# Kernel tuning notes

Hardware: AMD Instinct MI355X
Metric: run time of the kernel (lower is better)

## Reference

```python
import jax, jax.numpy as jnp
import numpy as np

NUM_USERS = 100000
NUM_ITEMS = 100000
DIM = 128
B = 8192
H = 200
ATTN_HID = 64


def setup_inputs() -> dict:
    key = jax.random.key(0)
    ks = jax.random.split(key, 10)
    user_ids = jax.random.randint(ks[0], (B,), 0, NUM_USERS)
    item_ids = jax.random.randint(ks[1], (B,), 0, NUM_ITEMS)
    user_history = jax.random.randint(ks[2], (B, H), 0, NUM_ITEMS)
    user_table = jax.random.normal(ks[3], (NUM_USERS, DIM), dtype=jnp.float32)
    item_table = jax.random.normal(ks[4], (NUM_ITEMS, DIM), dtype=jnp.float32)
    feature_interaction = jax.random.normal(ks[5], (DIM, DIM), dtype=jnp.float32)
    # attention MLP: Linear(2*DIM, 64) -> ReLU -> Linear(64, 1) -> Sigmoid
    lim1 = 1.0 / np.sqrt(2 * DIM)
    w1 = jax.random.uniform(ks[6], (2 * DIM, ATTN_HID), minval=-lim1, maxval=lim1, dtype=jnp.float32)
    b1 = jax.random.uniform(ks[7], (ATTN_HID,), minval=-lim1, maxval=lim1, dtype=jnp.float32)
    lim2 = 1.0 / np.sqrt(ATTN_HID)
    w2 = jax.random.uniform(ks[8], (ATTN_HID, 1), minval=-lim2, maxval=lim2, dtype=jnp.float32)
    b2 = jax.random.uniform(ks[9], (1,), minval=-lim2, maxval=lim2, dtype=jnp.float32)
    return {
        "user_ids": user_ids,
        "item_ids": item_ids,
        "user_history": user_history,
        "user_table": user_table,
        "item_table": item_table,
        "feature_interaction": feature_interaction,
        "w1": w1,
        "b1": b1,
        "w2": w2,
        "b2": b2,
    }


def reference(user_ids, item_ids, user_history, user_table, item_table,
              feature_interaction, w1, b1, w2, b2):
    user_emb = user_table[user_ids]          # [B, D]
    item_emb = item_table[item_ids]          # [B, D]
    # bilinear interaction: (user_emb @ W) . item_emb, summed over D -> [B, 1]
    interaction = jnp.sum((user_emb @ feature_interaction) * item_emb, axis=1, keepdims=True)
    # attention-weighted history pooling
    history_emb = item_table[user_history]   # [B, H, D]
    u = jnp.broadcast_to(user_emb[:, None, :], history_emb.shape)  # [B, H, D]
    attn_in = jnp.concatenate([u, history_emb], axis=-1)           # [B, H, 2D]
    h = jax.nn.relu(attn_in @ w1 + b1)                             # [B, H, 64]
    attn_w = jax.nn.sigmoid(h @ w2 + b2)                           # [B, H, 1]
    history_repr = jnp.sum(attn_w * history_emb, axis=1)           # [B, D]
    user_out = user_emb + history_repr
    return (user_out, item_emb, interaction)
```

## Files before the change

### kernel.cpp

```cpp
#include <hip/hip_runtime.h>
#include <math.h>

#define NB      8192
#define HLEN    200
#define DIM     128
#define AH      64
#define NITEMS  100000
#define WTILES  7
#define GATHER_BLKS (NB / 2)
#define INTER_BLKS  (NB / 4)
#define CONV_BLKS 1024

typedef __attribute__((ext_vector_type(4))) float f32x4;
typedef __attribute__((ext_vector_type(2))) float f32x2;
typedef __attribute__((ext_vector_type(4))) int   i32x4;
typedef __attribute__((ext_vector_type(8))) short bf16x8;
typedef unsigned int uint;

__device__ __forceinline__ unsigned short f2bf(float f) {
  uint u = __float_as_uint(f);
  u += 0x7fffu + ((u >> 16) & 1u);
  return (unsigned short)(u >> 16);
}
__device__ __forceinline__ float bf2f(unsigned short h) {
  return __uint_as_float(((uint)h) << 16);
}
__device__ __forceinline__ long pick64(const i32x4& v, int h) {
  return (long)(unsigned)v[2 * h] | ((long)(unsigned)v[2 * h + 1] << 32);
}

__global__ __launch_bounds__(256)
void conv_kernel(const float* __restrict__ item_table,
                 const float* __restrict__ w1,
                 unsigned char* __restrict__ tbl8,
                 unsigned char* __restrict__ w1f8) {
  const long t0 = (long)blockIdx.x * 256 + threadIdx.x;
  const long total4 = (long)NITEMS * DIM / 4;
  const long stride = (long)CONV_BLKS * 256;
  for (long i = t0; i < total4; i += stride) {
    f32x4 v = ((const f32x4*)item_table)[i];
    int p = __builtin_amdgcn_cvt_pk_fp8_f32(v[0], v[1], 0, false);
    p     = __builtin_amdgcn_cvt_pk_fp8_f32(v[2], v[3], p, true);
    ((int*)tbl8)[i] = p;
  }
  if (t0 < 16384) {
    int L = (int)t0;
    int j = L & 7, gg = (L >> 3) & 3, mm = (L >> 5) & 15;
    int nt = (L >> 9) & 3, s = (L >> 11) & 3, part = (L >> 13) & 1;
    int kg = part * 128 + (s >> 1) * 64 + gg * 16 + (s & 1) * 8 + j;
    float v = w1[kg * AH + nt * 16 + mm];
    int pk = __builtin_amdgcn_cvt_pk_fp8_f32(v, v, 0, false);
    w1f8[L] = (unsigned char)(pk & 0xff);
  }
}

__global__ __launch_bounds__(256)
void main_kernel_fp8(const int* __restrict__ user_ids,
                     const int* __restrict__ item_ids,
                     const int* __restrict__ user_history,
                     const float* __restrict__ user_table,
                     const float* __restrict__ item_table,
                     const float* __restrict__ fi,
                     const unsigned char* __restrict__ tbl8,
                     const unsigned char* __restrict__ w1f8,
                     const float* __restrict__ b1,
                     const float* __restrict__ w2,
                     const float* __restrict__ b2,
                     float* __restrict__ out_user,
                     float* __restrict__ out_item,
                     float* __restrict__ out_inter) {
  __shared__ __align__(16) unsigned char ldsbuf[35392];
  const int t = threadIdx.x;
  if (blockIdx.x < GATHER_BLKS) {
    float* comb = (float*)ldsbuf;
    const int lane = t & 63;
    const int wave = t >> 6;
    const int bslot = wave >> 1;
    const int h = wave & 1;
    const int b = blockIdx.x * 2 + bslot;
    const int m = lane & 15;
    const int g = lane >> 4;

    const int uid = __builtin_amdgcn_readfirstlane(user_ids[b]);
    const float* urow = user_table + (long)uid * DIM;
    const int* hrow = user_history + (long)b * HLEN;

    int idxs[WTILES];
#pragma unroll
    for (int tt = 0; tt < WTILES; ++tt) {
      int row = (h * WTILES + tt) * 16 + m;
      idxs[tt] = (row < HLEN) ? hrow[row] : 0;
    }

    i32x4 pa[4][2];
#define LOADT(T, BUF)                                                          \
    {                                                                          \
      const unsigned char* p_ = tbl8 + ((long)idxs[T] << 7) + g * 16;          \
      pa[BUF][0] = *(const i32x4*)p_;                                          \
      pa[BUF][1] = *(const i32x4*)(p_ + 64);                                   \
    }
    LOADT(0, 0) LOADT(1, 1) LOADT(2, 2)

    i32x4 uf[2];
#pragma unroll
    for (int kb = 0; kb < 2; ++kb) {
      const float* up = urow + kb * 64 + g * 16;
      f32x4 q0 = *(const f32x4*)(up + 0);
      f32x4 q1 = *(const f32x4*)(up + 4);
      f32x4 q2 = *(const f32x4*)(up + 8);
      f32x4 q3 = *(const f32x4*)(up + 12);
      i32x4 d;
      d[0] = __builtin_amdgcn_cvt_pk_fp8_f32(q0[0], q0[1], 0, false);
      d[0] = __builtin_amdgcn_cvt_pk_fp8_f32(q0[2], q0[3], d[0], true);
      d[1] = __builtin_amdgcn_cvt_pk_fp8_f32(q1[0], q1[1], 0, false);
      d[1] = __builtin_amdgcn_cvt_pk_fp8_f32(q1[2], q1[3], d[1], true);
      d[2] = __builtin_amdgcn_cvt_pk_fp8_f32(q2[0], q2[1], 0, false);
      d[2] = __builtin_amdgcn_cvt_pk_fp8_f32(q2[2], q2[3], d[2], true);
      d[3] = __builtin_amdgcn_cvt_pk_fp8_f32(q3[0], q3[1], 0, false);
      d[3] = __builtin_amdgcn_cvt_pk_fp8_f32(q3[2], q3[3], d[3], true);
      uf[kb] = d;
    }

    const unsigned char* wtop = w1f8;
    const unsigned char* wbot = w1f8 + 8192;

    f32x4 accu[4];
#pragma unroll
    for (int nt = 0; nt < 4; ++nt) accu[nt] = (f32x4){0.f, 0.f, 0.f, 0.f};
#pragma unroll
    for (int s = 0; s < 4; ++s) {
      long a_s = pick64(uf[s >> 1], s & 1);
#pragma unroll
      for (int nt = 0; nt < 4; ++nt) {
        long bf = *(const long*)(wtop + ((s * 4 + nt) * 16 + m) * 32 + g * 8);
        accu[nt] = __builtin_amdgcn_mfma_f32_16x16x32_fp8_fp8(a_s, bf, accu[nt], 0, 0, 0);
      }
    }
    float ubreg[4], w2reg[4];
#pragma unroll
    for (int nt = 0; nt < 4; ++nt) {
      ubreg[nt] = accu[nt][0] + b1[nt * 16 + m];
      w2reg[nt] = w2[nt * 16 + m];
    }
    const float b2v = b2[0];

    long bfr[4][4];
#pragma unroll
    for (int s = 0; s < 4; ++s)
#pragma unroll
      for (int nt = 0; nt < 4; ++nt)
        bfr[s][nt] = *(const long*)(wbot + ((s * 4 + nt) * 16 + m) * 32 + g * 8);

    float arep[32];
#pragma unroll
    for (int c = 0; c < 32; ++c) arep[c] = 0.f;

#pragma unroll
    for (int tt = 0; tt < WTILES; ++tt) {
      if (tt + 3 < WTILES) LOADT(tt + 3, (tt + 3) & 3)
      const int cb = tt & 3;

      f32x4 acc[4];
#pragma unroll
      for (int nt = 0; nt < 4; ++nt) acc[nt] = (f32x4){0.f, 0.f, 0.f, 0.f};
#pragma unroll
      for (int s = 0; s < 4; ++s) {
        long a_s = pick64(pa[cb][s >> 1], s & 1);
#pragma unroll
        for (int nt = 0; nt < 4; ++nt)
          acc[nt] = __builtin_amdgcn_mfma_f32_16x16x32_fp8_fp8(a_s, bfr[s][nt], acc[nt], 0, 0, 0);
      }

      float sums[4];
#pragma unroll
      for (int r = 0; r < 4; ++r) {
        float s = 0.f;
#pragma unroll
        for (int nt = 0; nt < 4; ++nt) {
          float hh = fmaxf(acc[nt][r] + ubreg[nt], 0.f);
          s = fmaf(hh, w2reg[nt], s);
        }
        s += __shfl_xor(s, 1);
        s += __shfl_xor(s, 2);
        s += __shfl_xor(s, 4);
        s += __shfl_xor(s, 8);
        sums[r] = s;
      }
      const int q = m & 3;
      float keep = (q == 0) ? sums[0] : (q == 1) ? sums[1] : (q == 2) ? sums[2] : sums[3];
      float sv = __shfl(keep, ((m >> 2) << 4) | m);
      float attw = 1.f / (1.f + __expf(-(sv + b2v)));
      if ((h * WTILES + tt) * 16 + m >= HLEN) attw = 0.f;

#pragma unroll
      for (int kb = 0; kb < 2; ++kb)
#pragma unroll
        for (int d = 0; d < 4; ++d) {
          f32x2 lo = __builtin_amdgcn_cvt_pk_f32_fp8(pa[cb][kb][d], false);
          f32x2 hi = __builtin_amdgcn_cvt_pk_f32_fp8(pa[cb][kb][d], true);
          const int base = kb * 16 + d * 4;
          arep[base + 0] = fmaf(attw, lo[0], arep[base + 0]);
          arep[base + 1] = fmaf(attw, lo[1], arep[base + 1]);
          arep[base + 2] = fmaf(attw, hi[0], arep[base + 2]);
          arep[base + 3] = fmaf(attw, hi[1], arep[base + 3]);
        }
    }
#undef LOADT

#pragma unroll
    for (int c = 0; c < 32; ++c) {
      arep[c] += __shfl_xor(arep[c], 1);
      arep[c] += __shfl_xor(arep[c], 2);
      arep[c] += __shfl_xor(arep[c], 4);
      arep[c] += __shfl_xor(arep[c], 8);
    }

    if (h == 1 && m == 0) {
#pragma unroll
      for (int kb = 0; kb < 2; ++kb)
#pragma unroll
        for (int i4 = 0; i4 < 4; ++i4)
#pragma unroll
          for (int qq = 0; qq < 4; ++qq)
            comb[bslot * 128 + kb * 64 + g * 16 + i4 * 4 + qq] = arep[kb * 16 + i4 * 4 + qq];
    }
    __syncthreads();
    if (h == 0 && m == 0) {
#pragma unroll
      for (int kb = 0; kb < 2; ++kb)
#pragma unroll
        for (int i4 = 0; i4 < 4; ++i4) {
          const int col = kb * 64 + g * 16 + i4 * 4;
          f32x4 uv = *(const f32x4*)(urow + col);
          f32x4 o;
#pragma unroll
          for (int qq = 0; qq < 4; ++qq)
            o[qq] = uv[qq] + arep[kb * 16 + i4 * 4 + qq] + comb[bslot * 128 + col + qq];
          *(f32x4*)(out_user + (long)b * DIM + col) = o;
        }
    }
  } else {
    unsigned short* fitb = (unsigned short*)ldsbuf;
    float (*u4)[DIM] = (float(*)[DIM])(ldsbuf + 33280);
    float (*red)[4] = (float(*)[4])(ldsbuf + 35328);
    for (int i = t; i < DIM * DIM; i += 256) {
      int d = i >> 7, e = i & 127;
      fitb[e * 130 + d] = f2bf(fi[i]);
    }
    const int col = t & 127;
    const int dh = t >> 7;
    const int lane = t & 63;
    const int wv = t >> 6;
    const int bb = (blockIdx.x - GATHER_BLKS) * 4;
    for (int i = t; i < 4 * DIM; i += 256) {
      int bi = i >> 7, d = i & 127;
      u4[bi][d] = user_table[(long)user_ids[bb + bi] * DIM + d];
    }
    __syncthreads();
    const unsigned short* fr = &fitb[col * 130 + dh * 64];
    float a0 = 0.f, a1 = 0.f, a2 = 0.f, a3 = 0.f;
#pragma unroll 4
    for (int d = 0; d < 64; d += 4) {
      float f0 = bf2f(fr[d]), f1 = bf2f(fr[d + 1]), f2 = bf2f(fr[d + 2]), f3 = bf2f(fr[d + 3]);
      f32x4 q0 = *(const f32x4*)&u4[0][dh * 64 + d];
      f32x4 q1 = *(const f32x4*)&u4[1][dh * 64 + d];
      f32x4 q2 = *(const f32x4*)&u4[2][dh * 64 + d];
      f32x4 q3 = *(const f32x4*)&u4[3][dh * 64 + d];
      a0 = fmaf(f0, q0[0], a0); a0 = fmaf(f1, q0[1], a0); a0 = fmaf(f2, q0[2], a0); a0 = fmaf(f3, q0[3], a0);
      a1 = fmaf(f0, q1[0], a1); a1 = fmaf(f1, q1[1], a1); a1 = fmaf(f2, q1[2], a1); a1 = fmaf(f3, q1[3], a1);
      a2 = fmaf(f0, q2[0], a2); a2 = fmaf(f1, q2[1], a2); a2 = fmaf(f2, q2[2], a2); a2 = fmaf(f3, q2[3], a2);
      a3 = fmaf(f0, q3[0], a3); a3 = fmaf(f1, q3[1], a3); a3 = fmaf(f2, q3[2], a3); a3 = fmaf(f3, q3[3], a3);
    }
    const float vv0 = item_table[(long)item_ids[bb + 0] * DIM + col];
    const float vv1 = item_table[(long)item_ids[bb + 1] * DIM + col];
    const float vv2 = item_table[(long)item_ids[bb + 2] * DIM + col];
    const float vv3 = item_table[(long)item_ids[bb + 3] * DIM + col];
    if (dh == 0) {
      out_item[(long)(bb + 0) * DIM + col] = vv0;
      out_item[(long)(bb + 1) * DIM + col] = vv1;
      out_item[(long)(bb + 2) * DIM + col] = vv2;
      out_item[(long)(bb + 3) * DIM + col] = vv3;
    }
    float p0 = a0 * vv0, p1 = a1 * vv1, p2 = a2 * vv2, p3 = a3 * vv3;
#pragma unroll
    for (int msk = 1; msk <= 32; msk <<= 1) {
      p0 += __shfl_xor(p0, msk);
      p1 += __shfl_xor(p1, msk);
      p2 += __shfl_xor(p2, msk);
      p3 += __shfl_xor(p3, msk);
    }
    if (lane == 0) { red[wv][0] = p0; red[wv][1] = p1; red[wv][2] = p2; red[wv][3] = p3; }
    __syncthreads();
    if (t < 4)
      out_inter[bb + t] = red[0][t] + red[1][t] + red[2][t] + red[3][t];
  }
}

__global__ __launch_bounds__(256)
void main_fallback(const int* __restrict__ user_ids,
                   const int* __restrict__ user_history,
                   const float* __restrict__ user_table,
                   const float* __restrict__ item_table,
                   const float* __restrict__ w1,
                   const float* __restrict__ b1,
                   const float* __restrict__ w2,
                   const float* __restrict__ b2,
                   float* __restrict__ out_user) {
  const int lane = threadIdx.x & 63;
  const int wave = threadIdx.x >> 6;
  const int b = blockIdx.x * 4 + wave;
  const int m = lane & 15, g = lane >> 4;
  const int uid = __builtin_amdgcn_readfirstlane(user_ids[b]);
  const float* urow = user_table + (long)uid * DIM;
  float upj = b1[lane];
#pragma unroll 8
  for (int d = 0; d < DIM; ++d) upj = fmaf(urow[d], w1[d * AH + lane], upj);
  bf16x8 bfr[4][4];
#pragma unroll
  for (int ks = 0; ks < 4; ++ks)
#pragma unroll
    for (int nt = 0; nt < 4; ++nt) {
      bf16x8 bv;
#pragma unroll
      for (int j = 0; j < 8; ++j)
        bv[j] = (short)f2bf(w1[(DIM + ks * 32 + g * 8 + j) * AH + nt * 16 + m]);
      bfr[ks][nt] = bv;
    }
  float ubreg[4], w2reg[4];
#pragma unroll
  for (int nt = 0; nt < 4; ++nt) {
    ubreg[nt] = __shfl(upj, nt * 16 + m);
    w2reg[nt] = w2[nt * 16 + m];
  }
  const float b2v = b2[0];
  float arep[32];
#pragma unroll
  for (int c = 0; c < 32; ++c) arep[c] = 0.f;
  const int* hrow = user_history + (long)b * HLEN;
  for (int tt = 0; tt < 13; ++tt) {
    const int row = tt * 16 + m;
    const int idx = (row < HLEN) ? hrow[row] : 0;
    bf16x8 a[4];
    const float* rp = item_table + (long)idx * DIM;
#pragma unroll
    for (int ks = 0; ks < 4; ++ks) {
      f32x4 lo = *(const f32x4*)(rp + ks * 32 + g * 8);
      f32x4 hi = *(const f32x4*)(rp + ks * 32 + g * 8 + 4);
      bf16x8 av;
      av[0] = (short)f2bf(lo[0]); av[1] = (short)f2bf(lo[1]);
      av[2] = (short)f2bf(lo[2]); av[3] = (short)f2bf(lo[3]);
      av[4] = (short)f2bf(hi[0]); av[5] = (short)f2bf(hi[1]);
      av[6] = (short)f2bf(hi[2]); av[7] = (short)f2bf(hi[3]);
      a[ks] = av;
    }
    f32x4 acc[4];
#pragma unroll
    for (int nt = 0; nt < 4; ++nt) acc[nt] = (f32x4){0.f, 0.f, 0.f, 0.f};
#pragma unroll
    for (int ks = 0; ks < 4; ++ks)
#pragma unroll
      for (int nt = 0; nt < 4; ++nt)
        acc[nt] = __builtin_amdgcn_mfma_f32_16x16x32_bf16(a[ks], bfr[ks][nt], acc[nt], 0, 0, 0);
    float sums[4];
#pragma unroll
    for (int r = 0; r < 4; ++r) {
      float s = 0.f;
#pragma unroll
      for (int nt = 0; nt < 4; ++nt) {
        float hh = fmaxf(acc[nt][r] + ubreg[nt], 0.f);
        s = fmaf(hh, w2reg[nt], s);
      }
      s += __shfl_xor(s, 1); s += __shfl_xor(s, 2);
      s += __shfl_xor(s, 4); s += __shfl_xor(s, 8);
      sums[r] = s;
    }
    const int q = m & 3;
    float keep = (q == 0) ? sums[0] : (q == 1) ? sums[1] : (q == 2) ? sums[2] : sums[3];
    float sv = __shfl(keep, ((m >> 2) << 4) | m);
    float attw = 1.f / (1.f + __expf(-(sv + b2v)));
    if (row >= HLEN) attw = 0.f;
#pragma unroll
    for (int ks = 0; ks < 4; ++ks)
#pragma unroll
      for (int j = 0; j < 8; ++j)
        arep[ks * 8 + j] = fmaf(attw, bf2f((unsigned short)a[ks][j]), arep[ks * 8 + j]);
  }
#pragma unroll
  for (int c = 0; c < 32; ++c) {
    arep[c] += __shfl_xor(arep[c], 1);
    arep[c] += __shfl_xor(arep[c], 2);
    arep[c] += __shfl_xor(arep[c], 4);
    arep[c] += __shfl_xor(arep[c], 8);
  }
  if (m == 0) {
#pragma unroll
    for (int ks = 0; ks < 4; ++ks)
#pragma unroll
      for (int j = 0; j < 8; ++j) {
        const int col = ks * 32 + g * 8 + j;
        out_user[(long)b * DIM + col] = urow[col] + arep[ks * 8 + j];
      }
  }
}

__global__ __launch_bounds__(256)
void inter_kernel(const int* __restrict__ user_ids,
                  const int* __restrict__ item_ids,
                  const float* __restrict__ user_table,
                  const float* __restrict__ item_table,
                  const float* __restrict__ fi,
                  float* __restrict__ out_item,
                  float* __restrict__ out_inter) {
  __shared__ unsigned short fitb[DIM * 130];
  __shared__ float u4[4][DIM];
  __shared__ float red[4][4];
  const int t = threadIdx.x;
  for (int i = t; i < DIM * DIM; i += 256) {
    int d = i >> 7, e = i & 127;
    fitb[e * 130 + d] = f2bf(fi[i]);
  }
  const int col = t & 127;
  const int dh = t >> 7;
  const int lane = t & 63;
  const int wv = t >> 6;
  const int bb = blockIdx.x * 4;
  for (int i = t; i < 4 * DIM; i += 256) {
    int bi = i >> 7, d = i & 127;
    u4[bi][d] = user_table[(long)user_ids[bb + bi] * DIM + d];
  }
  __syncthreads();
  const unsigned short* fr = &fitb[col * 130 + dh * 64];
  float a0 = 0.f, a1 = 0.f, a2 = 0.f, a3 = 0.f;
#pragma unroll 4
  for (int d = 0; d < 64; d += 4) {
    float f0 = bf2f(fr[d]), f1 = bf2f(fr[d + 1]), f2 = bf2f(fr[d + 2]), f3 = bf2f(fr[d + 3]);
    f32x4 q0 = *(const f32x4*)&u4[0][dh * 64 + d];
    f32x4 q1 = *(const f32x4*)&u4[1][dh * 64 + d];
    f32x4 q2 = *(const f32x4*)&u4[2][dh * 64 + d];
    f32x4 q3 = *(const f32x4*)&u4[3][dh * 64 + d];
    a0 = fmaf(f0, q0[0], a0); a0 = fmaf(f1, q0[1], a0); a0 = fmaf(f2, q0[2], a0); a0 = fmaf(f3, q0[3], a0);
    a1 = fmaf(f0, q1[0], a1); a1 = fmaf(f1, q1[1], a1); a1 = fmaf(f2, q1[2], a1); a1 = fmaf(f3, q1[3], a1);
    a2 = fmaf(f0, q2[0], a2); a2 = fmaf(f1, q2[1], a2); a2 = fmaf(f2, q2[2], a2); a2 = fmaf(f3, q2[3], a2);
    a3 = fmaf(f0, q3[0], a3); a3 = fmaf(f1, q3[1], a3); a3 = fmaf(f2, q3[2], a3); a3 = fmaf(f3, q3[3], a3);
  }
  const float vv0 = item_table[(long)item_ids[bb + 0] * DIM + col];
  const float vv1 = item_table[(long)item_ids[bb + 1] * DIM + col];
  const float vv2 = item_table[(long)item_ids[bb + 2] * DIM + col];
  const float vv3 = item_table[(long)item_ids[bb + 3] * DIM + col];
  if (dh == 0) {
    out_item[(long)(bb + 0) * DIM + col] = vv0;
    out_item[(long)(bb + 1) * DIM + col] = vv1;
    out_item[(long)(bb + 2) * DIM + col] = vv2;
    out_item[(long)(bb + 3) * DIM + col] = vv3;
  }
  float p0 = a0 * vv0, p1 = a1 * vv1, p2 = a2 * vv2, p3 = a3 * vv3;
#pragma unroll
  for (int msk = 1; msk <= 32; msk <<= 1) {
    p0 += __shfl_xor(p0, msk);
    p1 += __shfl_xor(p1, msk);
    p2 += __shfl_xor(p2, msk);
    p3 += __shfl_xor(p3, msk);
  }
  if (lane == 0) { red[wv][0] = p0; red[wv][1] = p1; red[wv][2] = p2; red[wv][3] = p3; }
  __syncthreads();
  if (t < 4)
    out_inter[bb + t] = red[0][t] + red[1][t] + red[2][t] + red[3][t];
}

extern "C" void kernel_launch(void* const* d_in, const int* in_sizes, int n_in,
                              void* d_out, int out_size, void* d_ws, size_t ws_size,
                              hipStream_t stream) {
  const int*   user_ids     = (const int*)d_in[0];
  const int*   item_ids     = (const int*)d_in[1];
  const int*   user_history = (const int*)d_in[2];
  const float* user_table   = (const float*)d_in[3];
  const float* item_table   = (const float*)d_in[4];
  const float* fi           = (const float*)d_in[5];
  const float* w1           = (const float*)d_in[6];
  const float* b1           = (const float*)d_in[7];
  const float* w2           = (const float*)d_in[8];
  const float* b2           = (const float*)d_in[9];

  float* out       = (float*)d_out;
  float* out_user  = out;
  float* out_item  = out + (size_t)NB * DIM;
  float* out_inter = out + (size_t)2 * NB * DIM;

  const size_t need = (size_t)NITEMS * DIM + 16384;
  if (ws_size >= need) {
    unsigned char* tbl8 = (unsigned char*)d_ws;
    unsigned char* w1f8 = tbl8 + (size_t)NITEMS * DIM;
    conv_kernel<<<CONV_BLKS, 256, 0, stream>>>(item_table, w1, tbl8, w1f8);
    main_kernel_fp8<<<GATHER_BLKS + INTER_BLKS, 256, 0, stream>>>(user_ids, item_ids,
        user_history, user_table, item_table, fi, tbl8, w1f8, b1, w2, b2,
        out_user, out_item, out_inter);
  } else {
    main_fallback<<<NB / 4, 256, 0, stream>>>(user_ids, user_history, user_table,
        item_table, w1, b1, w2, b2, out_user);
    inter_kernel<<<NB / 4, 256, 0, stream>>>(user_ids, item_ids, user_table,
        item_table, fi, out_item, out_inter);
  }
}
```

Measured before the change: 101.5 us.

## Partition history gather by item range so blocks hit localized table slices

The history pooling is split into four item-range partitions. Each block handles one partition for four batch rows, builds a compacted list of history slots whose item falls in that range, and writes bf16 partial sums that a new reduce kernel combines with the user embedding. The intent is to keep each block's fp8 table reads within a quarter of the table for better L2/MALL locality. The user-side attention projection (user_emb @ w1_top + b1) moves into the prep kernel as scalar FMA work, and the conversion and interaction work are fused into that prep launch. The cost is an extra kernel launch, a workspace round trip through bf16 partials that loses some precision, variable tile counts per wave, and a scalar, non-MFMA projection loop.

```diff
diff --git a/kernel.cpp b/kernel.cpp
--- a/kernel.cpp
+++ b/kernel.cpp
@@ -6,10 +6,10 @@
 #define DIM     128
 #define AH      64
 #define NITEMS  100000
-#define WTILES  7
-#define GATHER_BLKS (NB / 2)
-#define INTER_BLKS  (NB / 4)
+#define NPART   4
+#define PITEMS  25000
 #define CONV_BLKS 1024
+#define INTER_BLKS (NB / 4)
 
 typedef __attribute__((ext_vector_type(4))) float f32x4;
 typedef __attribute__((ext_vector_type(2))) float f32x2;
@@ -30,214 +30,47 @@
 }
 
 __global__ __launch_bounds__(256)
-void conv_kernel(const float* __restrict__ item_table,
+void prep_kernel(const int* __restrict__ user_ids,
+                 const int* __restrict__ item_ids,
+                 const float* __restrict__ user_table,
+                 const float* __restrict__ item_table,
+                 const float* __restrict__ fi,
                  const float* __restrict__ w1,
+                 const float* __restrict__ b1,
                  unsigned char* __restrict__ tbl8,
-                 unsigned char* __restrict__ w1f8) {
-  const long t0 = (long)blockIdx.x * 256 + threadIdx.x;
-  const long total4 = (long)NITEMS * DIM / 4;
-  const long stride = (long)CONV_BLKS * 256;
-  for (long i = t0; i < total4; i += stride) {
-    f32x4 v = ((const f32x4*)item_table)[i];
-    int p = __builtin_amdgcn_cvt_pk_fp8_f32(v[0], v[1], 0, false);
-    p     = __builtin_amdgcn_cvt_pk_fp8_f32(v[2], v[3], p, true);
-    ((int*)tbl8)[i] = p;
-  }
-  if (t0 < 16384) {
-    int L = (int)t0;
-    int j = L & 7, gg = (L >> 3) & 3, mm = (L >> 5) & 15;
-    int nt = (L >> 9) & 3, s = (L >> 11) & 3, part = (L >> 13) & 1;
-    int kg = part * 128 + (s >> 1) * 64 + gg * 16 + (s & 1) * 8 + j;
-    float v = w1[kg * AH + nt * 16 + mm];
-    int pk = __builtin_amdgcn_cvt_pk_fp8_f32(v, v, 0, false);
-    w1f8[L] = (unsigned char)(pk & 0xff);
-  }
-}
-
-__global__ __launch_bounds__(256)
-void main_kernel_fp8(const int* __restrict__ user_ids,
-                     const int* __restrict__ item_ids,
-                     const int* __restrict__ user_history,
-                     const float* __restrict__ user_table,
-                     const float* __restrict__ item_table,
-                     const float* __restrict__ fi,
-                     const unsigned char* __restrict__ tbl8,
-                     const unsigned char* __restrict__ w1f8,
-                     const float* __restrict__ b1,
-                     const float* __restrict__ w2,
-                     const float* __restrict__ b2,
-                     float* __restrict__ out_user,
-                     float* __restrict__ out_item,
-                     float* __restrict__ out_inter) {
+                 unsigned char* __restrict__ w1f8,
+                 float* __restrict__ ub,
+                 float* __restrict__ out_item,
+                 float* __restrict__ out_inter) {
   __shared__ __align__(16) unsigned char ldsbuf[35392];
   const int t = threadIdx.x;
-  if (blockIdx.x < GATHER_BLKS) {
-    float* comb = (float*)ldsbuf;
-    const int lane = t & 63;
-    const int wave = t >> 6;
-    const int bslot = wave >> 1;
-    const int h = wave & 1;
-    const int b = blockIdx.x * 2 + bslot;
-    const int m = lane & 15;
-    const int g = lane >> 4;
-
-    const int uid = __builtin_amdgcn_readfirstlane(user_ids[b]);
-    const float* urow = user_table + (long)uid * DIM;
-    const int* hrow = user_history + (long)b * HLEN;
-
-    int idxs[WTILES];
-#pragma unroll
-    for (int tt = 0; tt < WTILES; ++tt) {
-      int row = (h * WTILES + tt) * 16 + m;
-      idxs[tt] = (row < HLEN) ? hrow[row] : 0;
-    }
-
-    i32x4 pa[4][2];
-#define LOADT(T, BUF)                                                          \
-    {                                                                          \
-      const unsigned char* p_ = tbl8 + ((long)idxs[T] << 7) + g * 16;          \
-      pa[BUF][0] = *(const i32x4*)p_;                                          \
-      pa[BUF][1] = *(const i32x4*)(p_ + 64);                                   \
-    }
-    LOADT(0, 0) LOADT(1, 1) LOADT(2, 2)
-
-    i32x4 uf[2];
-#pragma unroll
-    for (int kb = 0; kb < 2; ++kb) {
-      const float* up = urow + kb * 64 + g * 16;
-      f32x4 q0 = *(const f32x4*)(up + 0);
-      f32x4 q1 = *(const f32x4*)(up + 4);
-      f32x4 q2 = *(const f32x4*)(up + 8);
-      f32x4 q3 = *(const f32x4*)(up + 12);
-      i32x4 d;
-      d[0] = __builtin_amdgcn_cvt_pk_fp8_f32(q0[0], q0[1], 0, false);
-      d[0] = __builtin_amdgcn_cvt_pk_fp8_f32(q0[2], q0[3], d[0], true);
-      d[1] = __builtin_amdgcn_cvt_pk_fp8_f32(q1[0], q1[1], 0, false);
-      d[1] = __builtin_amdgcn_cvt_pk_fp8_f32(q1[2], q1[3], d[1], true);
-      d[2] = __builtin_amdgcn_cvt_pk_fp8_f32(q2[0], q2[1], 0, false);
-      d[2] = __builtin_amdgcn_cvt_pk_fp8_f32(q2[2], q2[3], d[2], true);
-      d[3] = __builtin_amdgcn_cvt_pk_fp8_f32(q3[0], q3[1], 0, false);
-      d[3] = __builtin_amdgcn_cvt_pk_fp8_f32(q3[2], q3[3], d[3], true);
-      uf[kb] = d;
-    }
-
-    const unsigned char* wtop = w1f8;
-    const unsigned char* wbot = w1f8 + 8192;
-
-    f32x4 accu[4];
-#pragma unroll
-    for (int nt = 0; nt < 4; ++nt) accu[nt] = (f32x4){0.f, 0.f, 0.f, 0.f};
-#pragma unroll
-    for (int s = 0; s < 4; ++s) {
-      long a_s = pick64(uf[s >> 1], s & 1);
-#pragma unroll
-      for (int nt = 0; nt < 4; ++nt) {
-        long bf = *(const long*)(wtop + ((s * 4 + nt) * 16 + m) * 32 + g * 8);
-        accu[nt] = __builtin_amdgcn_mfma_f32_16x16x32_fp8_fp8(a_s, bf, accu[nt], 0, 0, 0);
-      }
-    }
-    float ubreg[4], w2reg[4];
-#pragma unroll
-    for (int nt = 0; nt < 4; ++nt) {
-      ubreg[nt] = accu[nt][0] + b1[nt * 16 + m];
-      w2reg[nt] = w2[nt * 16 + m];
-    }
-    const float b2v = b2[0];
-
-    long bfr[4][4];
-#pragma unroll
-    for (int s = 0; s < 4; ++s)
-#pragma unroll
-      for (int nt = 0; nt < 4; ++nt)
-        bfr[s][nt] = *(const long*)(wbot + ((s * 4 + nt) * 16 + m) * 32 + g * 8);
-
-    float arep[32];
-#pragma unroll
-    for (int c = 0; c < 32; ++c) arep[c] = 0.f;
-
-#pragma unroll
-    for (int tt = 0; tt < WTILES; ++tt) {
-      if (tt + 3 < WTILES) LOADT(tt + 3, (tt + 3) & 3)
-      const int cb = tt & 3;
-
-      f32x4 acc[4];
-#pragma unroll
-      for (int nt = 0; nt < 4; ++nt) acc[nt] = (f32x4){0.f, 0.f, 0.f, 0.f};
-#pragma unroll
-      for (int s = 0; s < 4; ++s) {
-        long a_s = pick64(pa[cb][s >> 1], s & 1);
-#pragma unroll
-        for (int nt = 0; nt < 4; ++nt)
-          acc[nt] = __builtin_amdgcn_mfma_f32_16x16x32_fp8_fp8(a_s, bfr[s][nt], acc[nt], 0, 0, 0);
-      }
-
-      float sums[4];
-#pragma unroll
-      for (int r = 0; r < 4; ++r) {
-        float s = 0.f;
-#pragma unroll
-        for (int nt = 0; nt < 4; ++nt) {
-          float hh = fmaxf(acc[nt][r] + ubreg[nt], 0.f);
-          s = fmaf(hh, w2reg[nt], s);
-        }
-        s += __shfl_xor(s, 1);
-        s += __shfl_xor(s, 2);
-        s += __shfl_xor(s, 4);
-        s += __shfl_xor(s, 8);
-        sums[r] = s;
-      }
-      const int q = m & 3;
-      float keep = (q == 0) ? sums[0] : (q == 1) ? sums[1] : (q == 2) ? sums[2] : sums[3];
-      float sv = __shfl(keep, ((m >> 2) << 4) | m);
-      float attw = 1.f / (1.f + __expf(-(sv + b2v)));
-      if ((h * WTILES + tt) * 16 + m >= HLEN) attw = 0.f;
-
-#pragma unroll
-      for (int kb = 0; kb < 2; ++kb)
-#pragma unroll
-        for (int d = 0; d < 4; ++d) {
-          f32x2 lo = __builtin_amdgcn_cvt_pk_f32_fp8(pa[cb][kb][d], false);
-          f32x2 hi = __builtin_amdgcn_cvt_pk_f32_fp8(pa[cb][kb][d], true);
-          const int base = kb * 16 + d * 4;
-          arep[base + 0] = fmaf(attw, lo[0], arep[base + 0]);
-          arep[base + 1] = fmaf(attw, lo[1], arep[base + 1]);
-          arep[base + 2] = fmaf(attw, hi[0], arep[base + 2]);
-          arep[base + 3] = fmaf(attw, hi[1], arep[base + 3]);
-        }
-    }
-#undef LOADT
-
-#pragma unroll
-    for (int c = 0; c < 32; ++c) {
-      arep[c] += __shfl_xor(arep[c], 1);
-      arep[c] += __shfl_xor(arep[c], 2);
-      arep[c] += __shfl_xor(arep[c], 4);
-      arep[c] += __shfl_xor(arep[c], 8);
-    }
-
-    if (h == 1 && m == 0) {
-#pragma unroll
-      for (int kb = 0; kb < 2; ++kb)
-#pragma unroll
-        for (int i4 = 0; i4 < 4; ++i4)
-#pragma unroll
-          for (int qq = 0; qq < 4; ++qq)
-            comb[bslot * 128 + kb * 64 + g * 16 + i4 * 4 + qq] = arep[kb * 16 + i4 * 4 + qq];
-    }
-    __syncthreads();
-    if (h == 0 && m == 0) {
-#pragma unroll
-      for (int kb = 0; kb < 2; ++kb)
-#pragma unroll
-        for (int i4 = 0; i4 < 4; ++i4) {
-          const int col = kb * 64 + g * 16 + i4 * 4;
-          f32x4 uv = *(const f32x4*)(urow + col);
-          f32x4 o;
-#pragma unroll
-          for (int qq = 0; qq < 4; ++qq)
-            o[qq] = uv[qq] + arep[kb * 16 + i4 * 4 + qq] + comb[bslot * 128 + col + qq];
-          *(f32x4*)(out_user + (long)b * DIM + col) = o;
-        }
+  if (blockIdx.x < CONV_BLKS) {
+    const long t0 = (long)blockIdx.x * 256 + t;
+    const long total4 = (long)NITEMS * DIM / 4;
+    const long stride = (long)CONV_BLKS * 256;
+    for (long i = t0; i < total4; i += stride) {
+      f32x4 v = ((const f32x4*)item_table)[i];
+      int p = __builtin_amdgcn_cvt_pk_fp8_f32(v[0], v[1], 0, false);
+      p     = __builtin_amdgcn_cvt_pk_fp8_f32(v[2], v[3], p, true);
+      ((int*)tbl8)[i] = p;
+    }
+    if (t0 < 16384) {
+      int L = (int)t0;
+      int j = L & 7, gg = (L >> 3) & 3, mm = (L >> 5) & 15;
+      int nt = (L >> 9) & 3, s = (L >> 11) & 3, part = (L >> 13) & 1;
+      int kg = part * 128 + (s >> 1) * 64 + gg * 16 + (s & 1) * 8 + j;
+      float v = w1[kg * AH + nt * 16 + mm];
+      int pk = __builtin_amdgcn_cvt_pk_fp8_f32(v, v, 0, false);
+      w1f8[L] = (unsigned char)(pk & 0xff);
+    }
+    for (long i = t0; i < (long)NB * AH; i += stride) {
+      int b = (int)(i >> 6), n = (int)(i & 63);
+      const float* urow = user_table + (long)user_ids[b] * DIM;
+      float acc = b1[n];
+#pragma unroll 8
+      for (int d = 0; d < DIM; ++d)
+        acc = fmaf(urow[d], w1[d * AH + n], acc);
+      ub[i] = acc;
     }
   } else {
     unsigned short* fitb = (unsigned short*)ldsbuf;
@@ -251,7 +84,7 @@
     const int dh = t >> 7;
     const int lane = t & 63;
     const int wv = t >> 6;
-    const int bb = (blockIdx.x - GATHER_BLKS) * 4;
+    const int bb = (blockIdx.x - CONV_BLKS) * 4;
     for (int i = t; i < 4 * DIM; i += 256) {
       int bi = i >> 7, d = i & 127;
       u4[bi][d] = user_table[(long)user_ids[bb + bi] * DIM + d];
@@ -294,6 +127,165 @@
     if (t < 4)
       out_inter[bb + t] = red[0][t] + red[1][t] + red[2][t] + red[3][t];
   }
+}
+
+__global__ __launch_bounds__(256)
+void gather_kernel(const int* __restrict__ user_ids,
+                   const int* __restrict__ user_history,
+                   const unsigned char* __restrict__ tbl8,
+                   const unsigned char* __restrict__ w1f8,
+                   const float* __restrict__ ub,
+                   const float* __restrict__ w2,
+                   const float* __restrict__ b2,
+                   unsigned short* __restrict__ partial) {
+  __shared__ unsigned char lists[4][256];
+  const int lane = threadIdx.x & 63;
+  const int wave = threadIdx.x >> 6;
+  const int p = blockIdx.x & 3;
+  const int b = (blockIdx.x >> 2) * 4 + wave;
+  const int m = lane & 15;
+  const int g = lane >> 4;
+  const int* hrow = user_history + (long)b * HLEN;
+
+  int cnt = 0;
+#pragma unroll
+  for (int c = 0; c < 4; ++c) {
+    const int slot = c * 64 + lane;
+    const bool vld = slot < HLEN;
+    int idx = 0;
+    if (vld) idx = hrow[slot];
+    const bool inp = vld && (idx / PITEMS == p);
+    unsigned long long mask = __ballot(inp);
+    int pos = cnt + __popcll(mask & ((1ull << lane) - 1ull));
+    if (inp) lists[wave][pos] = (unsigned char)slot;
+    cnt += (int)__popcll(mask);
+  }
+  __syncthreads();
+
+  const unsigned char* wbot = w1f8 + 8192;
+  long bfr[4][4];
+#pragma unroll
+  for (int s = 0; s < 4; ++s)
+#pragma unroll
+    for (int nt = 0; nt < 4; ++nt)
+      bfr[s][nt] = *(const long*)(wbot + ((s * 4 + nt) * 16 + m) * 32 + g * 8);
+  float ubreg[4], w2reg[4];
+#pragma unroll
+  for (int nt = 0; nt < 4; ++nt) {
+    ubreg[nt] = ub[(long)b * AH + nt * 16 + m];
+    w2reg[nt] = w2[nt * 16 + m];
+  }
+  const float b2v = b2[0];
+
+  float arep[32];
+#pragma unroll
+  for (int c = 0; c < 32; ++c) arep[c] = 0.f;
+
+  const int ntiles = (cnt + 15) >> 4;
+  for (int tt = 0; tt < ntiles; ++tt) {
+    const int j = tt * 16 + m;
+    const bool valid = j < cnt;
+    int idx = 0;
+    if (valid) idx = hrow[lists[wave][j]];
+    const unsigned char* rp = tbl8 + ((long)idx << 7) + g * 16;
+    i32x4 pa0 = *(const i32x4*)rp;
+    i32x4 pa1 = *(const i32x4*)(rp + 64);
+
+    f32x4 acc[4];
+#pragma unroll
+    for (int nt = 0; nt < 4; ++nt) acc[nt] = (f32x4){0.f, 0.f, 0.f, 0.f};
+#pragma unroll
+    for (int s = 0; s < 4; ++s) {
+      long a_s = pick64((s < 2) ? pa0 : pa1, s & 1);
+#pragma unroll
+      for (int nt = 0; nt < 4; ++nt)
+        acc[nt] = __builtin_amdgcn_mfma_f32_16x16x32_fp8_fp8(a_s, bfr[s][nt], acc[nt], 0, 0, 0);
+    }
+
+    float sums[4];
+#pragma unroll
+    for (int r = 0; r < 4; ++r) {
+      float s = 0.f;
+#pragma unroll
+      for (int nt = 0; nt < 4; ++nt) {
+        float hh = fmaxf(acc[nt][r] + ubreg[nt], 0.f);
+        s = fmaf(hh, w2reg[nt], s);
+      }
+      s += __shfl_xor(s, 1);
+      s += __shfl_xor(s, 2);
+      s += __shfl_xor(s, 4);
+      s += __shfl_xor(s, 8);
+      sums[r] = s;
+    }
+    const int q = m & 3;
+    float keep = (q == 0) ? sums[0] : (q == 1) ? sums[1] : (q == 2) ? sums[2] : sums[3];
+    float sv = __shfl(keep, ((m >> 2) << 4) | m);
+    float attw = 1.f / (1.f + __expf(-(sv + b2v)));
+    if (!valid) attw = 0.f;
+
+#pragma unroll
+    for (int kb = 0; kb < 2; ++kb) {
+      const i32x4 pav = kb ? pa1 : pa0;
+#pragma unroll
+      for (int d = 0; d < 4; ++d) {
+        f32x2 lo = __builtin_amdgcn_cvt_pk_f32_fp8(pav[d], false);
+        f32x2 hi = __builtin_amdgcn_cvt_pk_f32_fp8(pav[d], true);
+        const int base = kb * 16 + d * 4;
+        arep[base + 0] = fmaf(attw, lo[0], arep[base + 0]);
+        arep[base + 1] = fmaf(attw, lo[1], arep[base + 1]);
+        arep[base + 2] = fmaf(attw, hi[0], arep[base + 2]);
+        arep[base + 3] = fmaf(attw, hi[1], arep[base + 3]);
+      }
+    }
+  }
+
+#pragma unroll
+  for (int c = 0; c < 32; ++c) {
+    arep[c] += __shfl_xor(arep[c], 1);
+    arep[c] += __shfl_xor(arep[c], 2);
+    arep[c] += __shfl_xor(arep[c], 4);
+    arep[c] += __shfl_xor(arep[c], 8);
+  }
+  if (m == 0) {
+    unsigned short* pp = partial + ((long)b * NPART + p) * DIM;
+#pragma unroll
+    for (int kb = 0; kb < 2; ++kb)
+#pragma unroll
+      for (int i4 = 0; i4 < 4; ++i4) {
+        const int col = kb * 64 + g * 16 + i4 * 4;
+        uint w0 = (uint)f2bf(arep[kb * 16 + i4 * 4 + 0]) |
+                  ((uint)f2bf(arep[kb * 16 + i4 * 4 + 1]) << 16);
+        uint w1_ = (uint)f2bf(arep[kb * 16 + i4 * 4 + 2]) |
+                   ((uint)f2bf(arep[kb * 16 + i4 * 4 + 3]) << 16);
+        *(uint*)(pp + col) = w0;
+        *(uint*)(pp + col + 2) = w1_;
+      }
+  }
+}
+
+__global__ __launch_bounds__(256)
+void reduce_kernel(const int* __restrict__ user_ids,
+                   const float* __restrict__ user_table,
+                   const unsigned short* __restrict__ partial,
+                   float* __restrict__ out_user) {
+  const int lane = threadIdx.x & 63;
+  const int wave = threadIdx.x >> 6;
+  const int b = blockIdx.x * 4 + wave;
+  const int uid = __builtin_amdgcn_readfirstlane(user_ids[b]);
+  const float* urow = user_table + (long)uid * DIM;
+  const int col = lane * 2;
+  float s0 = 0.f, s1 = 0.f;
+#pragma unroll
+  for (int p = 0; p < NPART; ++p) {
+    uint v = *(const uint*)(partial + ((long)b * NPART + p) * DIM + col);
+    s0 += bf2f((unsigned short)(v & 0xffff));
+    s1 += bf2f((unsigned short)(v >> 16));
+  }
+  f32x2 uv = *(const f32x2*)(urow + col);
+  f32x2 o;
+  o[0] = uv[0] + s0;
+  o[1] = uv[1] + s1;
+  *(f32x2*)(out_user + (long)b * DIM + col) = o;
 }
 
 __global__ __launch_bounds__(256)
@@ -486,14 +478,22 @@
   float* out_item  = out + (size_t)NB * DIM;
   float* out_inter = out + (size_t)2 * NB * DIM;
 
-  const size_t need = (size_t)NITEMS * DIM + 16384;
+  const size_t tbl8_b    = (size_t)NITEMS * DIM;
+  const size_t w1f8_b    = 16384;
+  const size_t ub_b      = (size_t)NB * AH * 4;
+  const size_t partial_b = (size_t)NB * NPART * DIM * 2;
+  const size_t need = tbl8_b + w1f8_b + ub_b + partial_b;
+
   if (ws_size >= need) {
     unsigned char* tbl8 = (unsigned char*)d_ws;
-    unsigned char* w1f8 = tbl8 + (size_t)NITEMS * DIM;
-    conv_kernel<<<CONV_BLKS, 256, 0, stream>>>(item_table, w1, tbl8, w1f8);
-    main_kernel_fp8<<<GATHER_BLKS + INTER_BLKS, 256, 0, stream>>>(user_ids, item_ids,
-        user_history, user_table, item_table, fi, tbl8, w1f8, b1, w2, b2,
-        out_user, out_item, out_inter);
+    unsigned char* w1f8 = tbl8 + tbl8_b;
+    float* ub = (float*)(w1f8 + w1f8_b);
+    unsigned short* partial = (unsigned short*)((unsigned char*)ub + ub_b);
+    prep_kernel<<<CONV_BLKS + INTER_BLKS, 256, 0, stream>>>(user_ids, item_ids,
+        user_table, item_table, fi, w1, b1, tbl8, w1f8, ub, out_item, out_inter);
+    gather_kernel<<<NB, 256, 0, stream>>>(user_ids, user_history, tbl8, w1f8,
+        ub, w2, b2, partial);
+    reduce_kernel<<<NB / 4, 256, 0, stream>>>(user_ids, user_table, partial, out_user);
   } else {
     main_fallback<<<NB / 4, 256, 0, stream>>>(user_ids, user_history, user_table,
         item_table, w1, b1, w2, b2, out_user);
```

After: 159.4 us. 1.57x slower.

## Precompute user attention projection in conv kernel, one wave per batch row

Applied to the files above, without the earlier changes.

The user-half of the attention MLP (user_emb @ W1_top + b1) now runs as an FP32 scalar loop inside the conversion kernel and is stored in a workspace buffer, where before each block did it with FP8 MFMAs. The gather kernel now gives each wave a whole history of 13 tiles, so the LDS exchange and __syncthreads between two half-history waves go away. Gather and interaction blocks are interleaved by block-index parity. The trade-offs are extra workspace traffic, a longer serial loop per wave, and a scalar 128-term dot per output in the prologue kernel, which could add time before the main kernel starts.

```diff
diff --git a/kernel.cpp b/kernel.cpp
--- a/kernel.cpp
+++ b/kernel.cpp
@@ -6,10 +6,10 @@
 #define DIM     128
 #define AH      64
 #define NITEMS  100000
-#define WTILES  7
-#define GATHER_BLKS (NB / 2)
-#define INTER_BLKS  (NB / 4)
+#define NTILE   13
 #define CONV_BLKS 1024
+#define GB      (NB / 4)
+#define IB      (NB / 4)
 
 typedef __attribute__((ext_vector_type(4))) float f32x4;
 typedef __attribute__((ext_vector_type(2))) float f32x2;
@@ -30,10 +30,14 @@
 }
 
 __global__ __launch_bounds__(256)
-void conv_kernel(const float* __restrict__ item_table,
+void conv_kernel(const int* __restrict__ user_ids,
+                 const float* __restrict__ user_table,
+                 const float* __restrict__ item_table,
                  const float* __restrict__ w1,
+                 const float* __restrict__ b1,
                  unsigned char* __restrict__ tbl8,
-                 unsigned char* __restrict__ w1f8) {
+                 unsigned char* __restrict__ w1f8,
+                 float* __restrict__ ub) {
   const long t0 = (long)blockIdx.x * 256 + threadIdx.x;
   const long total4 = (long)NITEMS * DIM / 4;
   const long stride = (long)CONV_BLKS * 256;
@@ -52,32 +56,38 @@
     int pk = __builtin_amdgcn_cvt_pk_fp8_f32(v, v, 0, false);
     w1f8[L] = (unsigned char)(pk & 0xff);
   }
+  for (long i = t0; i < (long)NB * AH; i += stride) {
+    int b = (int)(i >> 6), n = (int)(i & 63);
+    const float* urow = user_table + (long)user_ids[b] * DIM;
+    float acc = b1[n];
+#pragma unroll 8
+    for (int d = 0; d < DIM; ++d)
+      acc = fmaf(urow[d], w1[d * AH + n], acc);
+    ub[i] = acc;
+  }
 }
 
 __global__ __launch_bounds__(256)
-void main_kernel_fp8(const int* __restrict__ user_ids,
-                     const int* __restrict__ item_ids,
-                     const int* __restrict__ user_history,
-                     const float* __restrict__ user_table,
-                     const float* __restrict__ item_table,
-                     const float* __restrict__ fi,
-                     const unsigned char* __restrict__ tbl8,
-                     const unsigned char* __restrict__ w1f8,
-                     const float* __restrict__ b1,
-                     const float* __restrict__ w2,
-                     const float* __restrict__ b2,
-                     float* __restrict__ out_user,
-                     float* __restrict__ out_item,
-                     float* __restrict__ out_inter) {
+void main_kernel(const int* __restrict__ user_ids,
+                 const int* __restrict__ item_ids,
+                 const int* __restrict__ user_history,
+                 const float* __restrict__ user_table,
+                 const float* __restrict__ item_table,
+                 const float* __restrict__ fi,
+                 const unsigned char* __restrict__ tbl8,
+                 const unsigned char* __restrict__ w1f8,
+                 const float* __restrict__ ub,
+                 const float* __restrict__ w2,
+                 const float* __restrict__ b2,
+                 float* __restrict__ out_user,
+                 float* __restrict__ out_item,
+                 float* __restrict__ out_inter) {
   __shared__ __align__(16) unsigned char ldsbuf[35392];
   const int t = threadIdx.x;
-  if (blockIdx.x < GATHER_BLKS) {
-    float* comb = (float*)ldsbuf;
+  if ((blockIdx.x & 1) == 0) {
     const int lane = t & 63;
     const int wave = t >> 6;
-    const int bslot = wave >> 1;
-    const int h = wave & 1;
-    const int b = blockIdx.x * 2 + bslot;
+    const int b = (int)(blockIdx.x >> 1) * 4 + wave;
     const int m = lane & 15;
     const int g = lane >> 4;
 
@@ -85,10 +95,10 @@
     const float* urow = user_table + (long)uid * DIM;
     const int* hrow = user_history + (long)b * HLEN;
 
-    int idxs[WTILES];
-#pragma unroll
-    for (int tt = 0; tt < WTILES; ++tt) {
-      int row = (h * WTILES + tt) * 16 + m;
+    int idxs[NTILE];
+#pragma unroll
+    for (int tt = 0; tt < NTILE; ++tt) {
+      int row = tt * 16 + m;
       idxs[tt] = (row < HLEN) ? hrow[row] : 0;
     }
 
@@ -101,63 +111,28 @@
     }
     LOADT(0, 0) LOADT(1, 1) LOADT(2, 2)
 
-    i32x4 uf[2];
-#pragma unroll
-    for (int kb = 0; kb < 2; ++kb) {
-      const float* up = urow + kb * 64 + g * 16;
-      f32x4 q0 = *(const f32x4*)(up + 0);
-      f32x4 q1 = *(const f32x4*)(up + 4);
-      f32x4 q2 = *(const f32x4*)(up + 8);
-      f32x4 q3 = *(const f32x4*)(up + 12);
-      i32x4 d;
-      d[0] = __builtin_amdgcn_cvt_pk_fp8_f32(q0[0], q0[1], 0, false);
-      d[0] = __builtin_amdgcn_cvt_pk_fp8_f32(q0[2], q0[3], d[0], true);
-      d[1] = __builtin_amdgcn_cvt_pk_fp8_f32(q1[0], q1[1], 0, false);
-      d[1] = __builtin_amdgcn_cvt_pk_fp8_f32(q1[2], q1[3], d[1], true);
-      d[2] = __builtin_amdgcn_cvt_pk_fp8_f32(q2[0], q2[1], 0, false);
-      d[2] = __builtin_amdgcn_cvt_pk_fp8_f32(q2[2], q2[3], d[2], true);
-      d[3] = __builtin_amdgcn_cvt_pk_fp8_f32(q3[0], q3[1], 0, false);
-      d[3] = __builtin_amdgcn_cvt_pk_fp8_f32(q3[2], q3[3], d[3], true);
-      uf[kb] = d;
-    }
-
-    const unsigned char* wtop = w1f8;
     const unsigned char* wbot = w1f8 + 8192;
-
-    f32x4 accu[4];
-#pragma unroll
-    for (int nt = 0; nt < 4; ++nt) accu[nt] = (f32x4){0.f, 0.f, 0.f, 0.f};
-#pragma unroll
-    for (int s = 0; s < 4; ++s) {
-      long a_s = pick64(uf[s >> 1], s & 1);
-#pragma unroll
-      for (int nt = 0; nt < 4; ++nt) {
-        long bf = *(const long*)(wtop + ((s * 4 + nt) * 16 + m) * 32 + g * 8);
-        accu[nt] = __builtin_amdgcn_mfma_f32_16x16x32_fp8_fp8(a_s, bf, accu[nt], 0, 0, 0);
-      }
-    }
-    float ubreg[4], w2reg[4];
-#pragma unroll
-    for (int nt = 0; nt < 4; ++nt) {
-      ubreg[nt] = accu[nt][0] + b1[nt * 16 + m];
-      w2reg[nt] = w2[nt * 16 + m];
-    }
-    const float b2v = b2[0];
-
     long bfr[4][4];
 #pragma unroll
     for (int s = 0; s < 4; ++s)
 #pragma unroll
       for (int nt = 0; nt < 4; ++nt)
         bfr[s][nt] = *(const long*)(wbot + ((s * 4 + nt) * 16 + m) * 32 + g * 8);
+    float ubreg[4], w2reg[4];
+#pragma unroll
+    for (int nt = 0; nt < 4; ++nt) {
+      ubreg[nt] = ub[(long)b * AH + nt * 16 + m];
+      w2reg[nt] = w2[nt * 16 + m];
+    }
+    const float b2v = b2[0];
 
     float arep[32];
 #pragma unroll
     for (int c = 0; c < 32; ++c) arep[c] = 0.f;
 
 #pragma unroll
-    for (int tt = 0; tt < WTILES; ++tt) {
-      if (tt + 3 < WTILES) LOADT(tt + 3, (tt + 3) & 3)
+    for (int tt = 0; tt < NTILE; ++tt) {
+      if (tt + 3 < NTILE) LOADT(tt + 3, (tt + 3) & 3)
       const int cb = tt & 3;
 
       f32x4 acc[4];
@@ -190,7 +165,7 @@
       float keep = (q == 0) ? sums[0] : (q == 1) ? sums[1] : (q == 2) ? sums[2] : sums[3];
       float sv = __shfl(keep, ((m >> 2) << 4) | m);
       float attw = 1.f / (1.f + __expf(-(sv + b2v)));
-      if ((h * WTILES + tt) * 16 + m >= HLEN) attw = 0.f;
+      if (tt * 16 + m >= HLEN) attw = 0.f;
 
 #pragma unroll
       for (int kb = 0; kb < 2; ++kb)
@@ -214,18 +189,7 @@
       arep[c] += __shfl_xor(arep[c], 4);
       arep[c] += __shfl_xor(arep[c], 8);
     }
-
-    if (h == 1 && m == 0) {
-#pragma unroll
-      for (int kb = 0; kb < 2; ++kb)
-#pragma unroll
-        for (int i4 = 0; i4 < 4; ++i4)
-#pragma unroll
-          for (int qq = 0; qq < 4; ++qq)
-            comb[bslot * 128 + kb * 64 + g * 16 + i4 * 4 + qq] = arep[kb * 16 + i4 * 4 + qq];
-    }
-    __syncthreads();
-    if (h == 0 && m == 0) {
+    if (m == 0) {
 #pragma unroll
       for (int kb = 0; kb < 2; ++kb)
 #pragma unroll
@@ -234,8 +198,7 @@
           f32x4 uv = *(const f32x4*)(urow + col);
           f32x4 o;
 #pragma unroll
-          for (int qq = 0; qq < 4; ++qq)
-            o[qq] = uv[qq] + arep[kb * 16 + i4 * 4 + qq] + comb[bslot * 128 + col + qq];
+          for (int qq = 0; qq < 4; ++qq) o[qq] = uv[qq] + arep[kb * 16 + i4 * 4 + qq];
           *(f32x4*)(out_user + (long)b * DIM + col) = o;
         }
     }
@@ -251,7 +214,7 @@
     const int dh = t >> 7;
     const int lane = t & 63;
     const int wv = t >> 6;
-    const int bb = (blockIdx.x - GATHER_BLKS) * 4;
+    const int bb = (int)(blockIdx.x >> 1) * 4;
     for (int i = t; i < 4 * DIM; i += 256) {
       int bi = i >> 7, d = i & 127;
       u4[bi][d] = user_table[(long)user_ids[bb + bi] * DIM + d];
@@ -337,7 +300,7 @@
 #pragma unroll
   for (int c = 0; c < 32; ++c) arep[c] = 0.f;
   const int* hrow = user_history + (long)b * HLEN;
-  for (int tt = 0; tt < 13; ++tt) {
+  for (int tt = 0; tt < NTILE; ++tt) {
     const int row = tt * 16 + m;
     const int idx = (row < HLEN) ? hrow[row] : 0;
     bf16x8 a[4];
@@ -486,13 +449,19 @@
   float* out_item  = out + (size_t)NB * DIM;
   float* out_inter = out + (size_t)2 * NB * DIM;
 
-  const size_t need = (size_t)NITEMS * DIM + 16384;
+  const size_t tbl8_b = (size_t)NITEMS * DIM;
+  const size_t w1f8_b = 16384;
+  const size_t ub_b   = (size_t)NB * AH * 4;
+  const size_t need = tbl8_b + w1f8_b + ub_b;
+
   if (ws_size >= need) {
     unsigned char* tbl8 = (unsigned char*)d_ws;
-    unsigned char* w1f8 = tbl8 + (size_t)NITEMS * DIM;
-    conv_kernel<<<CONV_BLKS, 256, 0, stream>>>(item_table, w1, tbl8, w1f8);
-    main_kernel_fp8<<<GATHER_BLKS + INTER_BLKS, 256, 0, stream>>>(user_ids, item_ids,
-        user_history, user_table, item_table, fi, tbl8, w1f8, b1, w2, b2,
+    unsigned char* w1f8 = tbl8 + tbl8_b;
+    float* ub = (float*)(w1f8 + w1f8_b);
+    conv_kernel<<<CONV_BLKS, 256, 0, stream>>>(user_ids, user_table, item_table,
+        w1, b1, tbl8, w1f8, ub);
+    main_kernel<<<GB + IB, 256, 0, stream>>>(user_ids, item_ids, user_history,
+        user_table, item_table, fi, tbl8, w1f8, ub, w2, b2,
         out_user, out_item, out_inter);
   } else {
     main_fallback<<<NB / 4, 256, 0, stream>>>(user_ids, user_history, user_table,
```

After: 141.2 us. 1.39x slower.
